# Performance work log

Measured on AMD Instinct MI355X. Metric: run time of the kernel, lower is better.

## Reference

```python
import jax, jax.numpy as jnp
import numpy as np

B, T, C = 48, 200, 53          # batch, timepoints, ICA components
E, H, A = 32, 64, 64            # embed dim, GRU hidden dim, attention hidden dim
C2 = C * C                      # 2809
E1 = round(0.05 * C2)           # gta_embed out = 140
E2 = round(0.5 * C2)            # gta_attend hidden = 1404
O = 2                           # output classes
BN_EPS = 1e-5


def setup_inputs() -> dict:
    key = jax.random.key(0)
    ks = jax.random.split(key, 24)
    n = lambda k, shape, s: jax.random.normal(k, shape, dtype=jnp.float32) * s
    return {
        "x": jax.random.normal(ks[0], (B, T, C), dtype=jnp.float32),
        "emb_w": n(ks[1], (E,), 0.3), "emb_b": n(ks[2], (E,), 0.1),
        "w_ih": n(ks[3], (3 * H, E), 0.12), "w_hh": n(ks[4], (3 * H, H), 0.12),
        "b_ih": n(ks[5], (3 * H,), 0.05), "b_hh": n(ks[6], (3 * H,), 0.05),
        "wq": n(ks[7], (A, H), 0.12), "bq": n(ks[8], (A,), 0.05),
        "wk": n(ks[9], (A, H), 0.12), "bk": n(ks[10], (A,), 0.05),
        "wv": n(ks[11], (H, H), 0.12), "bv": n(ks[12], (H,), 0.05),
        "u0": jax.random.normal(ks[13], (H,), dtype=jnp.float32),
        "w_g1": n(ks[14], (E1, C2), 0.02), "b_g1": n(ks[15], (E1,), 0.02),
        "bn_g": jnp.ones((E1,), jnp.float32), "bn_b": jnp.zeros((E1,), jnp.float32),
        "w_g2": n(ks[16], (E2, E1), 0.05), "b_g2": n(ks[17], (E2,), 0.05),
        "w_g3": n(ks[18], (1, E2), 0.02), "b_g3": n(ks[19], (1,), 0.02),
        "w_clf": n(ks[20], (O, C2), 0.02), "b_clf": jnp.zeros((O,), jnp.float32),
    }


def _normalize(v, eps=1e-12):
    return v / (jnp.linalg.norm(v) + eps)


def _gru_cell(x, h, w_ih, w_hh, b_ih, b_hh):
    # torch GRU cell math. x:(N,E) h:(N,H)
    gi = x @ w_ih.T + b_ih
    gh = h @ w_hh.T + b_hh
    i_r, i_z, i_n = jnp.split(gi, 3, axis=-1)
    h_r, h_z, h_n = jnp.split(gh, 3, axis=-1)
    r = jax.nn.sigmoid(i_r + h_r)
    z = jax.nn.sigmoid(i_z + h_z)
    n = jnp.tanh(i_n + r * h_n)
    return (1.0 - z) * n + z * h


def _forward(x, emb_w, emb_b, w_ih, w_hh, b_ih, b_hh, wq, bq, wk, bk, wv, bv, u0,
             w_g1, b_g1, bn_g, bn_b, w_g2, b_g2, w_g3, b_g3, w_clf, b_clf):
    Bs, Ts, Cs = x.shape
    Hd = wv.shape[0]
    # single shared Linear(1,E) embedding: (B,T,C) -> (T,B,C,E) for scan
    emb = x[..., None] * emb_w + emb_b
    emb = jnp.transpose(emb, (1, 0, 2, 3))
    h0 = jnp.zeros((Bs * Cs, Hd), x.dtype)

    def step(carry, emb_t):
        h, u = carry
        hg = _gru_cell(emb_t.reshape(Bs * Cs, -1), h, w_ih, w_hh, b_ih, b_hh)
        hb = hg.reshape(Bs, Cs, Hd)
        # spectral_norm on value weight: 5 power iterations (no_grad, as torch)
        v = None
        for _ in range(5):
            v = _normalize(wv.T @ u)
            u = _normalize(wv @ v)
        u = jax.lax.stop_gradient(u)
        v = jax.lax.stop_gradient(v)
        sigma = u @ (wv @ v)
        q = hb @ wq.T + bq          # (B,C,A)
        k = hb @ wk.T + bk          # (B,C,A)
        val = hb @ (wv / sigma).T + bv  # (B,C,H)
        scores = jnp.einsum('bia,bja->bij', q, k)  # (B,C,C)
        # eigenvalue-based spectral normalization (detached: track_grads=False)
        ev = jnp.linalg.eigvals(jax.lax.stop_gradient(scores))
        m = jnp.max(jnp.abs(ev), axis=1)[:, None, None].astype(x.dtype)
        attn = scores / m
        h_new = jnp.einsum('bij,bjh->bih', attn, val).reshape(Bs * Cs, Hd)
        return (h_new, u), attn

    (_, _), aligns = jax.lax.scan(step, (h0, u0), emb)  # aligns: (T,B,C,C)
    align = jnp.transpose(aligns, (1, 0, 2, 3))         # (B,T,C,C)
    Aflat = align.reshape(Bs, Ts, Cs * Cs)

    # gta_attention over the time axis
    xr = Aflat * Aflat.mean(axis=1, keepdims=True)
    flat = xr.reshape(Bs * Ts, Cs * Cs)
    e = flat @ w_g1.T + b_g1
    mu = e.mean(axis=0)
    var = e.var(axis=0)  # biased, as torch BatchNorm1d (training)
    e = jax.nn.relu((e - mu) / jnp.sqrt(var + BN_EPS) * bn_g + bn_b)
    a = jax.nn.relu(e @ w_g2.T + b_g2) @ w_g3.T + b_g3   # (B*T,1)
    a = jax.nn.softmax(a.reshape(Bs, Ts), axis=1)
    dnc = (Aflat * a[..., None]).sum(axis=1)             # (B,C*C)
    logits = dnc @ w_clf.T + b_clf
    return logits, dnc.reshape(Bs, Cs, Cs), align


def reference(x, emb_w, emb_b, w_ih, w_hh, b_ih, b_hh, wq, bq, wk, bk, wv, bv, u0,
              w_g1, b_g1, bn_g, bn_b, w_g2, b_g2, w_g3, b_g3, w_clf, b_clf):
    return _forward(x, emb_w, emb_b, w_ih, w_hh, b_ih, b_hh, wq, bq, wk, bk, wv, bv, u0,
                    w_g1, b_g1, bn_g, bn_b, w_g2, b_g2, w_g3, b_g3, w_clf, b_clf)
```

## Files before the change

kernel.cpp:

```cpp
#include <hip/hip_runtime.h>
#include <hip/hip_bf16.h>
#include <math.h>

#define B_  48
#define T_  200
#define C_  53
#define H_  64
#define C2_ 2809
#define E1_ 140
#define E2_ 1404
#define TS  60

typedef long long i64;

struct __align__(16) F4 { float v[4]; };
struct __align__(8)  F2 { float v[2]; };

__device__ __forceinline__ float wredsum(float v){
  #pragma unroll
  for (int o = 32; o > 0; o >>= 1) v += __shfl_xor(v, o);
  return v;
}
__device__ __forceinline__ float sigm(float x){ return 1.f/(1.f + __expf(-x)); }
__device__ __forceinline__ float tanhx(float x){
  float a = fabsf(x);
  float e = __expf(-2.f*a);
  float t = (1.f - e)/(1.f + e);
  return copysignf(t, x);
}

__device__ __forceinline__ void eig_mm(const float* __restrict__ X, float* __restrict__ Y,
                                       int r0, int c0, float inv,
                                       float& essq, float& etrc){
  float ea0[4] = {0.f,0.f,0.f,0.f};
  float ea1[4] = {0.f,0.f,0.f,0.f};
  for (int kq = 0; kq < 13; kq++){
    int k4 = kq*4;
    F4 a0 = *(const F4*)&X[(r0+0)*TS + k4];
    F4 a1 = *(const F4*)&X[(r0+1)*TS + k4];
    F4 b0 = *(const F4*)&X[(k4+0)*TS + c0];
    F4 b1 = *(const F4*)&X[(k4+1)*TS + c0];
    F4 b2 = *(const F4*)&X[(k4+2)*TS + c0];
    F4 b3 = *(const F4*)&X[(k4+3)*TS + c0];
    #pragma unroll
    for (int ci = 0; ci < 4; ci++){
      ea0[ci] += a0.v[0]*b0.v[ci] + a0.v[1]*b1.v[ci] + a0.v[2]*b2.v[ci] + a0.v[3]*b3.v[ci];
      ea1[ci] += a1.v[0]*b0.v[ci] + a1.v[1]*b1.v[ci] + a1.v[2]*b2.v[ci] + a1.v[3]*b3.v[ci];
    }
  }
  {
    float a0 = X[(r0+0)*TS + 52], a1 = X[(r0+1)*TS + 52];
    F4 bb = *(const F4*)&X[52*TS + c0];
    #pragma unroll
    for (int ci = 0; ci < 4; ci++){ ea0[ci] += a0*bb.v[ci]; ea1[ci] += a1*bb.v[ci]; }
  }
  F4 o0, o1;
  #pragma unroll
  for (int ci = 0; ci < 4; ci++){
    o0.v[ci] = ea0[ci]*inv;
    o1.v[ci] = ea1[ci]*inv;
    essq += o0.v[ci]*o0.v[ci] + o1.v[ci]*o1.v[ci];
  }
  if (r0   >= c0 && r0   < c0+4) etrc += o0.v[r0-c0];
  if (r0+1 >= c0 && r0+1 < c0+4) etrc += o1.v[r0+1-c0];
  *(F4*)&Y[(r0+0)*TS + c0] = o0;
  *(F4*)&Y[(r0+1)*TS + c0] = o1;
}

#define OFF_SIGMA 0
#define OFF_WHHT  200
#define OFF_WZV   12488
#define OFF_WUV   20680
#define OFF_P     20812
#define OFF_R0    21004
#define OFF_MM    21196
#define OFF_M2    25292
#define OFF_M4    29388
#define OFF_M5    33484
#define OFF_AMEAN 37580
#define OFF_E     172412
#define OFF_CA    1516412
#define OFF_CB    1516552
#define OFF_APRE  1516692
#define OFF_A     1526292
#define OFF_G2T   1535892

__global__ void k_prep1(const float* __restrict__ w_hh, const float* __restrict__ wq,
                        const float* __restrict__ wk, const float* __restrict__ wv,
                        const float* __restrict__ w_ih, const float* __restrict__ emb_w,
                        const float* __restrict__ emb_b, const float* __restrict__ b_ih,
                        const float* __restrict__ bq, const float* __restrict__ bk,
                        const float* __restrict__ w_g2,
                        float* whhT, float* wzv, float* wuv, float* g2t,
                        float* p, float* r0){
  int idx0 = blockIdx.x*blockDim.x + threadIdx.x;
  int stride = gridDim.x*blockDim.x;
  for (int i = idx0; i < 64*192; i += stride){
    int kk = i/192, g = i%192;
    whhT[i] = w_hh[g*64 + kk];
  }
  for (int i = idx0; i < 8192; i += stride){
    int h = i >> 7, a = i & 127;
    if (a < 64){
      float g = 0.f;
      for (int m = 0; m < 64; m++) g += wq[m*64 + h]*wk[m*64 + a];
      wzv[i] = g;
    } else {
      wzv[i] = wv[(a-64)*64 + h];
    }
  }
  for (int i = idx0; i < 129; i += stride){
    if (i < 64){
      float s = 0.f;
      for (int m = 0; m < 64; m++) s += wq[m*64 + i]*bk[m];
      wuv[i] = s;
    } else if (i < 128){
      int h = i - 64;
      float s = 0.f;
      for (int m = 0; m < 64; m++) s += wk[m*64 + h]*bq[m];
      wuv[i] = s;
    } else {
      float s = 0.f;
      for (int m = 0; m < 64; m++) s += bq[m]*bk[m];
      wuv[128] = s;
    }
  }
  for (int i = idx0; i < 140*1404; i += stride){ int k = i/1404, n = i%1404; g2t[i] = w_g2[n*140+k]; }
  for (int i = idx0; i < 192; i += stride){
    float s1 = 0.f, s2 = 0.f;
    for (int e = 0; e < 32; e++){ float w = w_ih[i*32+e]; s1 += w*emb_w[e]; s2 += w*emb_b[e]; }
    p[i] = s1; r0[i] = s2 + b_ih[i];
  }
}

__global__ void k_prep2(const float* __restrict__ wv, const float* __restrict__ u0,
                        float* Wm, float* Wm2, float* Wm4, float* Wm5, float* sigma){
  int r = threadIdx.x;
  for (int c = 0; c < 64; c++){
    float s = 0.f;
    for (int k = 0; k < 64; k++) s += wv[r*64+k]*wv[c*64+k];
    Wm[r*64+c] = s;
  }
  __syncthreads();
  for (int c = 0; c < 64; c++){
    float s = 0.f;
    for (int k = 0; k < 64; k++) s += Wm[r*64+k]*Wm[k*64+c];
    Wm2[r*64+c] = s;
  }
  __syncthreads();
  for (int c = 0; c < 64; c++){
    float s = 0.f;
    for (int k = 0; k < 64; k++) s += Wm2[r*64+k]*Wm2[k*64+c];
    Wm4[r*64+c] = s;
  }
  __syncthreads();
  for (int c = 0; c < 64; c++){
    float s = 0.f;
    for (int k = 0; k < 64; k++) s += Wm4[r*64+k]*Wm[k*64+c];
    Wm5[r*64+c] = s;
  }
  __syncthreads();
  __shared__ float su[64];
  su[r] = u0[r];
  __syncthreads();
  for (int t = 0; t < T_; t++){
    float z = 0.f, w = 0.f;
    for (int k = 0; k < 64; k++){ float uk = su[k]; z += Wm4[r*64+k]*uk; w += Wm5[r*64+k]*uk; }
    float nw = wredsum(w*w);
    float zw = wredsum(z*w);
    float sg = sqrtf(nw / fmaxf(zw, 1e-35f));
    if (r == 0) sigma[t] = sg;
    float wn = w * (1.f/sqrtf(fmaxf(nw, 1e-35f)));
    __syncthreads();
    su[r] = wn;
    __syncthreads();
  }
}

__global__ __launch_bounds__(512, 1) void k_scan(
    const float* __restrict__ x, const float* __restrict__ b_hh,
    const float* __restrict__ bv,
    const float* __restrict__ whhT, const float* __restrict__ wzv,
    const float* __restrict__ wuv,
    const float* __restrict__ wp, const float* __restrict__ wr0,
    const float* __restrict__ sigma, float* __restrict__ outAL){
  __shared__ __align__(16) float L[19056];
  float* Rh  = L;
  float* R4  = L + 3840;
  float* R3  = L + 7680;
  float* R2  = L + 11520;
  float* R1  = L + 14912;
  float* Lp  = L + 18272;
  float* Lr0 = L + 18464;
  float* Lbh = L + 18656;
  float* Lbv = L + 18848;
  float* Lrq = L + 18912;
  float* Lrk = L + 18968;
  float* Lsc = L + 19024;
  int tid = threadIdx.x;
  int b = blockIdx.x;

  for (int i = tid; i < 192; i += 512){ Lp[i] = wp[i]; Lr0[i] = wr0[i]; Lbh[i] = b_hh[i]; }
  for (int i = tid; i < 64; i += 512) Lbv[i] = bv[i];
  for (int i = tid; i < 18272; i += 512) L[i] = 0.f;
  __syncthreads();

  int ct4 = tid >> 4, jt4 = tid & 15;
  int c0g = ct4*4, j0g = jt4*4;
  int it14 = tid/14, jt14 = tid%14;
  int i0s = it14*4, j0s = jt14*4;
  int ctq = tid >> 5, gtq = tid & 31;
  int c0q = ctq*4, g0q = gtq*4;
  int erg = tid/14, ecg = tid%14;
  int er0 = erg*2, ec0 = ecg*4;

  const float c0v = wuv[128];

  for (int t = 0; t < T_; t++){
    if (tid < 32) Lsc[tid] = 0.f;
    if (tid < 224){
      float gacc[3][4][4];
      #pragma unroll
      for (int g = 0; g < 3; g++)
        #pragma unroll
        for (int ji = 0; ji < 4; ji++){
          float bb = Lbh[g*64 + j0g + ji];
          #pragma unroll
          for (int ci = 0; ci < 4; ci++) gacc[g][ji][ci] = bb;
        }
      for (int kk = 0; kk < 64; kk++){
        F4 hv = *(F4*)&Rh[kk*TS + c0g];
        F4 w0 = *(const F4*)&whhT[kk*192 + j0g];
        F4 w1 = *(const F4*)&whhT[kk*192 + 64 + j0g];
        F4 w2 = *(const F4*)&whhT[kk*192 + 128 + j0g];
        #pragma unroll
        for (int ji = 0; ji < 4; ji++)
          #pragma unroll
          for (int ci = 0; ci < 4; ci++){
            gacc[0][ji][ci] += hv.v[ci]*w0.v[ji];
            gacc[1][ji][ci] += hv.v[ci]*w1.v[ji];
            gacc[2][ji][ci] += hv.v[ci]*w2.v[ji];
          }
      }
      float xv[4];
      #pragma unroll
      for (int ci = 0; ci < 4; ci++){
        int c = c0g + ci;
        xv[ci] = (c < C_) ? x[(i64)(b*T_ + t)*C_ + c] : 0.f;
      }
      F4 p0 = *(F4*)&Lp[j0g], p1 = *(F4*)&Lp[64+j0g], p2 = *(F4*)&Lp[128+j0g];
      F4 q0 = *(F4*)&Lr0[j0g], q1 = *(F4*)&Lr0[64+j0g], q2 = *(F4*)&Lr0[128+j0g];
      #pragma unroll
      for (int ji = 0; ji < 4; ji++){
        F4 hold = *(F4*)&Rh[(j0g+ji)*TS + c0g];
        F4 o;
        #pragma unroll
        for (int ci = 0; ci < 4; ci++){
          float rr = sigm(xv[ci]*p0.v[ji] + q0.v[ji] + gacc[0][ji][ci]);
          float zz = sigm(xv[ci]*p1.v[ji] + q1.v[ji] + gacc[1][ji][ci]);
          float nn = tanhx(xv[ci]*p2.v[ji] + q2.v[ji] + rr*gacc[2][ji][ci]);
          float hg = (1.f - zz)*nn + zz*hold.v[ci];
          o.v[ci] = (c0g + ci < C_) ? hg : 0.f;
        }
        *(F4*)&R4[(j0g+ji)*TS + c0g] = o;
      }
    }
    __syncthreads();
    if (tid < 448){
      float acc[4][4];
      #pragma unroll
      for (int gi = 0; gi < 4; gi++)
        #pragma unroll
        for (int ci = 0; ci < 4; ci++) acc[gi][ci] = 0.f;
      for (int kk = 0; kk < 64; kk++){
        F4 a = *(F4*)&R4[kk*TS + c0q];
        F4 w = *(const F4*)&wzv[kk*128 + g0q];
        #pragma unroll
        for (int gi = 0; gi < 4; gi++)
          #pragma unroll
          for (int ci = 0; ci < 4; ci++) acc[gi][ci] += a.v[ci]*w.v[gi];
      }
      if (g0q < 64){
        #pragma unroll
        for (int gi = 0; gi < 4; gi++){
          F4 o;
          #pragma unroll
          for (int ci = 0; ci < 4; ci++) o.v[ci] = acc[gi][ci];
          *(F4*)&R3[(g0q+gi)*TS + c0q] = o;
        }
      } else {
        float invs = 1.f/sigma[t];
        int a0i = g0q - 64;
        #pragma unroll
        for (int ci = 0; ci < 4; ci++){
          int c = c0q + ci;
          if (c < C_){
            F4 o;
            #pragma unroll
            for (int gi = 0; gi < 4; gi++) o.v[gi] = acc[gi][ci]*invs + Lbv[a0i+gi];
            *(F4*)&R2[c*64 + a0i] = o;
          }
        }
      }
    } else if (tid < 504){
      int u = tid - 448;
      float rq = 0.f, rk = 0.f;
      if (u < C_){
        for (int h = 0; h < 64; h++){
          float hv = R4[h*TS + u];
          rq += hv*wuv[h];
          rk += hv*wuv[64+h];
        }
      }
      if (u < 56){ Lrq[u] = rq; Lrk[u] = rk; }
    }
    __syncthreads();
    {
      float sacc[4][4];
      float ssq = 0.f, trc = 0.f;
      if (tid < 196){
        #pragma unroll
        for (int ii = 0; ii < 4; ii++)
          #pragma unroll
          for (int jj = 0; jj < 4; jj++){
            int i = i0s + ii, j = j0s + jj;
            sacc[ii][jj] = (i < C_ && j < C_) ? (Lrq[i] + Lrk[j] + c0v) : 0.f;
          }
        for (int aq = 0; aq < 16; aq++){
          int a4 = aq*4;
          F4 qa0 = *(F4*)&R3[(a4+0)*TS + i0s];
          F4 qa1 = *(F4*)&R3[(a4+1)*TS + i0s];
          F4 qa2 = *(F4*)&R3[(a4+2)*TS + i0s];
          F4 qa3 = *(F4*)&R3[(a4+3)*TS + i0s];
          F4 kb0 = *(F4*)&R4[(a4+0)*TS + j0s];
          F4 kb1 = *(F4*)&R4[(a4+1)*TS + j0s];
          F4 kb2 = *(F4*)&R4[(a4+2)*TS + j0s];
          F4 kb3 = *(F4*)&R4[(a4+3)*TS + j0s];
          #pragma unroll
          for (int ii = 0; ii < 4; ii++)
            #pragma unroll
            for (int jj = 0; jj < 4; jj++)
              sacc[ii][jj] += qa0.v[ii]*kb0.v[jj] + qa1.v[ii]*kb1.v[jj]
                            + qa2.v[ii]*kb2.v[jj] + qa3.v[ii]*kb3.v[jj];
        }
        #pragma unroll
        for (int ii = 0; ii < 4; ii++){
          int i = i0s + ii;
          if (i < C_){
            F4 o;
            #pragma unroll
            for (int jj = 0; jj < 4; jj++){
              o.v[jj] = sacc[ii][jj];
              ssq += sacc[ii][jj]*sacc[ii][jj];
            }
            *(F4*)&R1[i*TS + j0s] = o;
            if (j0s <= i && i < j0s + 4) trc += sacc[ii][i - j0s];
          }
        }
      }
      ssq = wredsum(ssq); trc = wredsum(trc);
      if ((tid & 63) == 0){
        if (ssq != 0.f) atomicAdd(&Lsc[0], ssq);
        if (trc != 0.f) atomicAdd(&Lsc[1], trc);
      }
    }
    __syncthreads();
    {
      float inv0 = 1.f/fmaxf(Lsc[0], 1e-35f);
      float essq = 0.f, etrc = 0.f;
      if (tid < 378) eig_mm(R1, R3, er0, ec0, inv0, essq, etrc);
      essq = wredsum(essq); etrc = wredsum(etrc);
      if ((tid & 63) == 0){
        if (essq != 0.f) atomicAdd(&Lsc[2], essq);
        if (etrc != 0.f) atomicAdd(&Lsc[3], etrc);
      }
    }
    __syncthreads();
    float Gacc = 0.f, prevest = 1e30f, est = 0.f;
    int cnt = 0;
    float pssq = fmaxf(Lsc[0], 1e-35f), ptr1 = Lsc[1];
    float* Xb = R3; float* Yb = R4;
    for (int j = 2; j <= 13; j++){
      float sj = fmaxf(Lsc[2*(j-1)], 1e-35f);
      float tj = Lsc[2*(j-1)+1];
      int J = j - 2;
      float t1n = ptr1/sqrtf(pssq);
      float t2n = tj;
      float disc = 2.f*t2n - t1n*t1n;
      float rq = (disc >= 0.f) ? 0.5f*(fabsf(t1n) + sqrtf(disc))
                               : sqrtf(fmaxf(0.5f*(t1n*t1n - t2n), 1e-30f));
      rq = fminf(fmaxf(rq, 0.02f), 1.5f);
      est = Gacc + ldexpf(0.5f*log2f(pssq) + log2f(rq), -J);
      if (fabsf(est - prevest) < 1e-4f) cnt++; else cnt = 0;
      prevest = est;
      Gacc += ldexpf(log2f(pssq), -(J+1));
      if ((J >= 4 && cnt >= 1) || j == 13) break;
      pssq = sj; ptr1 = tj;
      {
        float inv = 1.f/sj;
        float essq = 0.f, etrc = 0.f;
        if (tid < 378) eig_mm(Xb, Yb, er0, ec0, inv, essq, etrc);
        essq = wredsum(essq); etrc = wredsum(etrc);
        if ((tid & 63) == 0){
          if (essq != 0.f) atomicAdd(&Lsc[2*j], essq);
          if (etrc != 0.f) atomicAdd(&Lsc[2*j+1], etrc);
        }
      }
      { float* tp = Xb; Xb = Yb; Yb = tp; }
      __syncthreads();
    }
    float invm = exp2f(-est);
    if (tid < 224){
      float hraw0[4] = {0.f,0.f,0.f,0.f};
      float hraw1[4] = {0.f,0.f,0.f,0.f};
      float hraw2[4] = {0.f,0.f,0.f,0.f};
      float hraw3[4] = {0.f,0.f,0.f,0.f};
      for (int kq = 0; kq < 13; kq++){
        int k4 = kq*4;
        F4 a0 = *(F4*)&R1[(c0g+0)*TS + k4];
        F4 a1 = *(F4*)&R1[(c0g+1)*TS + k4];
        F4 a2 = *(F4*)&R1[(c0g+2)*TS + k4];
        F4 a3 = *(F4*)&R1[(c0g+3)*TS + k4];
        F4 b0 = *(F4*)&R2[(k4+0)*64 + j0g];
        F4 b1 = *(F4*)&R2[(k4+1)*64 + j0g];
        F4 b2 = *(F4*)&R2[(k4+2)*64 + j0g];
        F4 b3 = *(F4*)&R2[(k4+3)*64 + j0g];
        #pragma unroll
        for (int jj = 0; jj < 4; jj++){
          hraw0[jj] += a0.v[0]*b0.v[jj] + a0.v[1]*b1.v[jj] + a0.v[2]*b2.v[jj] + a0.v[3]*b3.v[jj];
          hraw1[jj] += a1.v[0]*b0.v[jj] + a1.v[1]*b1.v[jj] + a1.v[2]*b2.v[jj] + a1.v[3]*b3.v[jj];
          hraw2[jj] += a2.v[0]*b0.v[jj] + a2.v[1]*b1.v[jj] + a2.v[2]*b2.v[jj] + a2.v[3]*b3.v[jj];
          hraw3[jj] += a3.v[0]*b0.v[jj] + a3.v[1]*b1.v[jj] + a3.v[2]*b2.v[jj] + a3.v[3]*b3.v[jj];
        }
      }
      {
        const int k = 52;
        float a0 = R1[(c0g+0)*TS + k], a1 = R1[(c0g+1)*TS + k];
        float a2 = R1[(c0g+2)*TS + k], a3 = R1[(c0g+3)*TS + k];
        F4 bb = *(F4*)&R2[k*64 + j0g];
        #pragma unroll
        for (int jj = 0; jj < 4; jj++){
          hraw0[jj] += a0*bb.v[jj];
          hraw1[jj] += a1*bb.v[jj];
          hraw2[jj] += a2*bb.v[jj];
          hraw3[jj] += a3*bb.v[jj];
        }
      }
      #pragma unroll
      for (int jj = 0; jj < 4; jj++){
        F4 o;
        o.v[0] = (c0g + 0 < C_) ? hraw0[jj]*invm : 0.f;
        o.v[1] = (c0g + 1 < C_) ? hraw1[jj]*invm : 0.f;
        o.v[2] = (c0g + 2 < C_) ? hraw2[jj]*invm : 0.f;
        o.v[3] = (c0g + 3 < C_) ? hraw3[jj]*invm : 0.f;
        *(F4*)&Rh[(j0g+jj)*TS + c0g] = o;
      }
    } else if (tid < 420){
      int u = tid - 224;
      int i0 = (u/14)*4, j0 = (u%14)*4;
      float* ALrow = outAL + (i64)(b*T_ + t)*C2_;
      #pragma unroll
      for (int ii = 0; ii < 4; ii++){
        int i = i0 + ii;
        if (i < C_){
          F4 s = *(F4*)&R1[i*TS + j0];
          #pragma unroll
          for (int jj = 0; jj < 4; jj++){
            int jc = j0 + jj;
            if (jc < C_) ALrow[i*C_ + jc] = s.v[jj]*invm;
          }
        }
      }
    }
    __syncthreads();
  }
}

__global__ void k_amean(const float* __restrict__ AL, float* __restrict__ amean){
  int b = blockIdx.x/11, ch = blockIdx.x%11;
  int c2 = ch*256 + threadIdx.x;
  if (c2 >= C2_) return;
  float acc = 0.f;
  for (int t = 0; t < T_; t++)
    acc += AL[(i64)(b*T_ + t)*C2_ + c2];
  amean[(i64)b*C2_ + c2] = acc*(1.f/(float)T_);
}

__global__ __launch_bounds__(256) void k_gemm1(const float* __restrict__ AL,
                                               const float* __restrict__ amean,
                                               const float* __restrict__ w_g1,
                                               float* __restrict__ e){
  __shared__ __align__(16) float At[64][68];
  __shared__ __align__(16) float Bt[64][148];
  int mt = blockIdx.x >> 2, ks = blockIdx.x & 3;
  int tid = threadIdx.x;
  float acc[4][10];
  #pragma unroll
  for (int ri = 0; ri < 4; ri++)
    #pragma unroll
    for (int ci = 0; ci < 10; ci++) acc[ri][ci] = 0.f;
  int rg = tid/14, cg = tid%14;
  int r0 = rg*4, cc0 = cg*10;
  for (int kb = 0; kb < 11; kb++){
    int k0 = (ks*11 + kb)*64;
    for (int idx = tid; idx < 4096; idx += 256){
      int r = idx >> 6, i = idx & 63;
      int kk = k0 + i;
      int row = mt*64 + r, bb = row/T_;
      float v = 0.f;
      if (kk < C2_) v = AL[(i64)row*C2_ + kk]*amean[(i64)bb*C2_ + kk];
      At[i][r] = v;
    }
    for (int idx = tid; idx < 9216; idx += 256){
      int c = idx >> 6, i = idx & 63;
      int kk = k0 + i;
      float v = 0.f;
      if (c < E1_ && kk < C2_) v = w_g1[(i64)c*C2_ + kk];
      Bt[i][c] = v;
    }
    __syncthreads();
    if (tid < 224){
      for (int i = 0; i < 64; i++){
        F4 a = *(F4*)&At[i][r0];
        float bv[10];
        #pragma unroll
        for (int u = 0; u < 5; u++){
          F2 b2 = *(F2*)&Bt[i][cc0 + u*2];
          bv[u*2] = b2.v[0]; bv[u*2+1] = b2.v[1];
        }
        #pragma unroll
        for (int ri = 0; ri < 4; ri++)
          #pragma unroll
          for (int ci = 0; ci < 10; ci++)
            acc[ri][ci] += a.v[ri]*bv[ci];
      }
    }
    __syncthreads();
  }
  if (tid < 224){
    #pragma unroll
    for (int ri = 0; ri < 4; ri++)
      #pragma unroll
      for (int ci = 0; ci < 10; ci++){
        int c = cc0 + ci;
        if (c < E1_) atomicAdd(&e[(i64)(mt*64 + r0 + ri)*E1_ + c], acc[ri][ci]);
      }
  }
}

__global__ void k_bnstats(const float* __restrict__ e, const float* __restrict__ bn_g,
                          const float* __restrict__ bn_b, float* cA, float* cB){
  __shared__ float s1a[256], s2a[256];
  int c = blockIdx.x, tid = threadIdx.x;
  float s1 = 0.f, s2 = 0.f;
  for (int row = tid; row < B_*T_; row += 256){
    float v = e[(i64)row*E1_ + c];
    s1 += v; s2 += v*v;
  }
  s1a[tid] = s1; s2a[tid] = s2; __syncthreads();
  for (int s = 128; s > 0; s >>= 1){
    if (tid < s){ s1a[tid] += s1a[tid+s]; s2a[tid] += s2a[tid+s]; }
    __syncthreads();
  }
  if (tid == 0){
    float n = (float)(B_*T_);
    float mu = s1a[0]/n;
    float var = s2a[0]/n - mu*mu;
    float a = bn_g[c]/sqrtf(var + 1e-5f);
    cA[c] = a; cB[c] = bn_b[c] - mu*a;
  }
}

__global__ __launch_bounds__(128) void k_gemm2(const float* __restrict__ e,
                                               const float* __restrict__ cA, const float* __restrict__ cB,
                                               const float* __restrict__ g2t,
                                               const float* __restrict__ b_g2, const float* __restrict__ w_g3,
                                               float* __restrict__ apre){
  __shared__ __align__(16) float At2[140][68];
  int mt = blockIdx.x/30, nc = blockIdx.x%30;
  int tid = threadIdx.x;
  int nbase = nc*48;
  for (int idx = tid; idx < 64*140; idx += 128){
    int r = idx/140, k = idx - r*140;
    float v = e[(i64)(mt*64 + r)*E1_ + k]*cA[k] + cB[k];
    At2[k][r] = fmaxf(v, 0.f);
  }
  __syncthreads();
  if (tid < 96){
    int rg = tid/6, ng = tid%6;
    int r0 = rg*4, n0 = nbase + ng*8;
    float acc[4][8];
    #pragma unroll
    for (int ri = 0; ri < 4; ri++)
      #pragma unroll
      for (int ni = 0; ni < 8; ni++) acc[ri][ni] = 0.f;
    for (int k = 0; k < E1_; k++){
      F4 a = *(F4*)&At2[k][r0];
      float bvv[8];
      if (n0 + 8 <= E2_){
        F4 b0 = *(const F4*)&g2t[(i64)k*E2_ + n0];
        F4 b1 = *(const F4*)&g2t[(i64)k*E2_ + n0 + 4];
        #pragma unroll
        for (int u = 0; u < 4; u++){ bvv[u] = b0.v[u]; bvv[u+4] = b1.v[u]; }
      } else {
        #pragma unroll
        for (int ni = 0; ni < 8; ni++){ int n = n0+ni; bvv[ni] = (n < E2_) ? g2t[(i64)k*E2_ + n] : 0.f; }
      }
      #pragma unroll
      for (int ri = 0; ri < 4; ri++)
        #pragma unroll
        for (int ni = 0; ni < 8; ni++) acc[ri][ni] += a.v[ri]*bvv[ni];
    }
    #pragma unroll
    for (int ri = 0; ri < 4; ri++){
      float s = 0.f;
      #pragma unroll
      for (int ni = 0; ni < 8; ni++){
        int n = n0 + ni;
        if (n < E2_){
          float a2 = acc[ri][ni] + b_g2[n];
          if (a2 > 0.f) s += a2*w_g3[n];
        }
      }
      atomicAdd(&apre[mt*64 + r0 + ri], s);
    }
  }
}

__global__ void k_soft(const float* __restrict__ apre, const float* __restrict__ b_clf,
                       float* __restrict__ wa, float* __restrict__ out){
  __shared__ float sr[256];
  int b = blockIdx.x, tid = threadIdx.x;
  float v = (tid < T_) ? apre[b*T_ + tid] : -3.4e38f;
  sr[tid] = v; __syncthreads();
  for (int s = 128; s > 0; s >>= 1){ if (tid < s) sr[tid] = fmaxf(sr[tid], sr[tid+s]); __syncthreads(); }
  float mx = sr[0]; __syncthreads();
  float ev = (tid < T_) ? __expf(v - mx) : 0.f;
  sr[tid] = ev; __syncthreads();
  for (int s = 128; s > 0; s >>= 1){ if (tid < s) sr[tid] += sr[tid+s]; __syncthreads(); }
  float den = sr[0];
  if (tid < T_) wa[b*T_ + tid] = ev/den;
  if (b == 0 && tid < 2*B_) out[tid] = b_clf[tid & 1];
}

__global__ void k_dnc(const float* __restrict__ AL, const float* __restrict__ wa,
                      const float* __restrict__ w_clf, float* __restrict__ out){
  int b = blockIdx.x/11, ch = blockIdx.x%11;
  int c2 = ch*256 + threadIdx.x;
  float acc = 0.f;
  if (c2 < C2_){
    for (int t = 0; t < T_; t++)
      acc += AL[(i64)(b*T_ + t)*C2_ + c2]*wa[b*T_ + t];
    out[96 + (i64)b*C2_ + c2] = acc;
  }
  float p0 = (c2 < C2_) ? acc*w_clf[c2]        : 0.f;
  float p1 = (c2 < C2_) ? acc*w_clf[C2_ + c2]  : 0.f;
  p0 = wredsum(p0); p1 = wredsum(p1);
  if ((threadIdx.x & 63) == 0){
    atomicAdd(&out[b*2 + 0], p0);
    atomicAdd(&out[b*2 + 1], p1);
  }
}

extern "C" void kernel_launch(void* const* d_in, const int* in_sizes, int n_in,
                              void* d_out, int out_size, void* d_ws, size_t ws_size,
                              hipStream_t stream){
  const float* x     = (const float*)d_in[0];
  const float* emb_w = (const float*)d_in[1];
  const float* emb_b = (const float*)d_in[2];
  const float* w_ih  = (const float*)d_in[3];
  const float* w_hh  = (const float*)d_in[4];
  const float* b_ih  = (const float*)d_in[5];
  const float* b_hh  = (const float*)d_in[6];
  const float* wq    = (const float*)d_in[7];
  const float* bq    = (const float*)d_in[8];
  const float* wk    = (const float*)d_in[9];
  const float* bk    = (const float*)d_in[10];
  const float* wv_in = (const float*)d_in[11];
  const float* bv    = (const float*)d_in[12];
  const float* u0    = (const float*)d_in[13];
  const float* w_g1  = (const float*)d_in[14];
  const float* bn_g  = (const float*)d_in[16];
  const float* bn_b  = (const float*)d_in[17];
  const float* w_g2  = (const float*)d_in[18];
  const float* b_g2  = (const float*)d_in[19];
  const float* w_g3  = (const float*)d_in[20];
  const float* w_clf = (const float*)d_in[22];
  const float* b_clf = (const float*)d_in[23];
  float* out = (float*)d_out;
  float* W = (float*)d_ws;

  float* wsig   = W + OFF_SIGMA;
  float* whhT   = W + OFF_WHHT;
  float* wzv    = W + OFF_WZV;
  float* wuv    = W + OFF_WUV;
  float* wp     = W + OFF_P;
  float* wr0    = W + OFF_R0;
  float* wM     = W + OFF_MM;
  float* wM2    = W + OFF_M2;
  float* wM4    = W + OFF_M4;
  float* wM5    = W + OFF_M5;
  float* wamean = W + OFF_AMEAN;
  float* we     = W + OFF_E;
  float* wcA    = W + OFF_CA;
  float* wcB    = W + OFF_CB;
  float* wapre  = W + OFF_APRE;
  float* wa     = W + OFF_A;
  float* wg2t   = W + OFF_G2T;

  float* outAL = out + 96 + (i64)B_*C2_;

  hipMemsetAsync(we, 0, (size_t)(B_*T_)*E1_*sizeof(float), stream);
  hipMemsetAsync(wapre, 0, (size_t)(B_*T_)*sizeof(float), stream);

  k_prep1<<<96, 256, 0, stream>>>(w_hh, wq, wk, wv_in, w_ih, emb_w, emb_b, b_ih, bq, bk,
                                  w_g2, whhT, wzv, wuv, wg2t, wp, wr0);
  k_prep2<<<1, 64, 0, stream>>>(wv_in, u0, wM, wM2, wM4, wM5, wsig);
  k_scan<<<B_, 512, 0, stream>>>(x, b_hh, bv, whhT, wzv, wuv, wp, wr0, wsig, outAL);
  k_amean<<<B_*11, 256, 0, stream>>>(outAL, wamean);
  k_gemm1<<<600, 256, 0, stream>>>(outAL, wamean, w_g1, we);
  k_bnstats<<<E1_, 256, 0, stream>>>(we, bn_g, bn_b, wcA, wcB);
  k_gemm2<<<150*30, 128, 0, stream>>>(we, wcA, wcB, wg2t, b_g2, w_g3, wapre);
  k_soft<<<B_, 256, 0, stream>>>(wapre, b_clf, wa, out);
  k_dnc<<<B_*11, 256, 0, stream>>>(outAL, wa, w_clf, out);
}
```

Baseline: 8.720 ms.

## Overlap unscaled attention-value matmul with first eigen-step and loosen convergence check

The first eigen squaring matmul is remapped to 252 threads with 3x4 tiles. The freed threads run the attention-times-value product (R1·R2) concurrently, before the normalising scale is known, and that product is later rescaled in place by invm. This takes the value matmul off the serial path after the log-norm iteration. The convergence test now allows an early break one iteration sooner (J>=3), which saves an eigen step but may slightly change the estimate's accuracy.

```diff
diff --git a/kernel.cpp b/kernel.cpp
--- a/kernel.cpp
+++ b/kernel.cpp
@@ -65,6 +65,52 @@
   if (r0+1 >= c0 && r0+1 < c0+4) etrc += o1.v[r0+1-c0];
   *(F4*)&Y[(r0+0)*TS + c0] = o0;
   *(F4*)&Y[(r0+1)*TS + c0] = o1;
+}
+
+__device__ __forceinline__ void eig_mm3(const float* __restrict__ X, float* __restrict__ Y,
+                                        int r0, int c0, float inv,
+                                        float& essq, float& etrc){
+  float ea0[4] = {0.f,0.f,0.f,0.f};
+  float ea1[4] = {0.f,0.f,0.f,0.f};
+  float ea2[4] = {0.f,0.f,0.f,0.f};
+  for (int kq = 0; kq < 13; kq++){
+    int k4 = kq*4;
+    F4 a0 = *(const F4*)&X[(r0+0)*TS + k4];
+    F4 a1 = *(const F4*)&X[(r0+1)*TS + k4];
+    F4 a2 = *(const F4*)&X[(r0+2)*TS + k4];
+    F4 b0 = *(const F4*)&X[(k4+0)*TS + c0];
+    F4 b1 = *(const F4*)&X[(k4+1)*TS + c0];
+    F4 b2 = *(const F4*)&X[(k4+2)*TS + c0];
+    F4 b3 = *(const F4*)&X[(k4+3)*TS + c0];
+    #pragma unroll
+    for (int ci = 0; ci < 4; ci++){
+      ea0[ci] += a0.v[0]*b0.v[ci] + a0.v[1]*b1.v[ci] + a0.v[2]*b2.v[ci] + a0.v[3]*b3.v[ci];
+      ea1[ci] += a1.v[0]*b0.v[ci] + a1.v[1]*b1.v[ci] + a1.v[2]*b2.v[ci] + a1.v[3]*b3.v[ci];
+      ea2[ci] += a2.v[0]*b0.v[ci] + a2.v[1]*b1.v[ci] + a2.v[2]*b2.v[ci] + a2.v[3]*b3.v[ci];
+    }
+  }
+  {
+    float a0 = X[(r0+0)*TS + 52], a1 = X[(r0+1)*TS + 52], a2 = X[(r0+2)*TS + 52];
+    F4 bb = *(const F4*)&X[52*TS + c0];
+    #pragma unroll
+    for (int ci = 0; ci < 4; ci++){
+      ea0[ci] += a0*bb.v[ci]; ea1[ci] += a1*bb.v[ci]; ea2[ci] += a2*bb.v[ci];
+    }
+  }
+  F4 o0, o1, o2;
+  #pragma unroll
+  for (int ci = 0; ci < 4; ci++){
+    o0.v[ci] = ea0[ci]*inv;
+    o1.v[ci] = ea1[ci]*inv;
+    o2.v[ci] = ea2[ci]*inv;
+    essq += o0.v[ci]*o0.v[ci] + o1.v[ci]*o1.v[ci] + o2.v[ci]*o2.v[ci];
+  }
+  if (r0   >= c0 && r0   < c0+4) etrc += o0.v[r0-c0];
+  if (r0+1 >= c0 && r0+1 < c0+4) etrc += o1.v[r0+1-c0];
+  if (r0+2 >= c0 && r0+2 < c0+4) etrc += o2.v[r0+2-c0];
+  *(F4*)&Y[(r0+0)*TS + c0] = o0;
+  *(F4*)&Y[(r0+1)*TS + c0] = o1;
+  *(F4*)&Y[(r0+2)*TS + c0] = o2;
 }
 
 #define OFF_SIGMA 0
@@ -366,9 +412,59 @@
     }
     __syncthreads();
     {
-      float inv0 = 1.f/fmaxf(Lsc[0], 1e-35f);
       float essq = 0.f, etrc = 0.f;
-      if (tid < 378) eig_mm(R1, R3, er0, ec0, inv0, essq, etrc);
+      if (tid < 252){
+        float inv0 = 1.f/fmaxf(Lsc[0], 1e-35f);
+        int r0e = (tid/14)*3, c0e = (tid%14)*4;
+        eig_mm3(R1, R3, r0e, c0e, inv0, essq, etrc);
+      } else if (tid < 476){
+        int u = tid - 252;
+        int c0 = (u >> 4)*4, j0 = (u & 15)*4;
+        float hr0[4] = {0.f,0.f,0.f,0.f};
+        float hr1[4] = {0.f,0.f,0.f,0.f};
+        float hr2[4] = {0.f,0.f,0.f,0.f};
+        float hr3[4] = {0.f,0.f,0.f,0.f};
+        for (int kq = 0; kq < 13; kq++){
+          int k4 = kq*4;
+          F4 a0 = *(F4*)&R1[(c0+0)*TS + k4];
+          F4 a1 = *(F4*)&R1[(c0+1)*TS + k4];
+          F4 a2 = *(F4*)&R1[(c0+2)*TS + k4];
+          F4 a3 = *(F4*)&R1[(c0+3)*TS + k4];
+          F4 b0 = *(F4*)&R2[(k4+0)*64 + j0];
+          F4 b1 = *(F4*)&R2[(k4+1)*64 + j0];
+          F4 b2 = *(F4*)&R2[(k4+2)*64 + j0];
+          F4 b3 = *(F4*)&R2[(k4+3)*64 + j0];
+          #pragma unroll
+          for (int jj = 0; jj < 4; jj++){
+            hr0[jj] += a0.v[0]*b0.v[jj] + a0.v[1]*b1.v[jj] + a0.v[2]*b2.v[jj] + a0.v[3]*b3.v[jj];
+            hr1[jj] += a1.v[0]*b0.v[jj] + a1.v[1]*b1.v[jj] + a1.v[2]*b2.v[jj] + a1.v[3]*b3.v[jj];
+            hr2[jj] += a2.v[0]*b0.v[jj] + a2.v[1]*b1.v[jj] + a2.v[2]*b2.v[jj] + a2.v[3]*b3.v[jj];
+            hr3[jj] += a3.v[0]*b0.v[jj] + a3.v[1]*b1.v[jj] + a3.v[2]*b2.v[jj] + a3.v[3]*b3.v[jj];
+          }
+        }
+        {
+          const int k = 52;
+          float a0 = R1[(c0+0)*TS + k], a1 = R1[(c0+1)*TS + k];
+          float a2 = R1[(c0+2)*TS + k], a3 = R1[(c0+3)*TS + k];
+          F4 bb = *(F4*)&R2[k*64 + j0];
+          #pragma unroll
+          for (int jj = 0; jj < 4; jj++){
+            hr0[jj] += a0*bb.v[jj];
+            hr1[jj] += a1*bb.v[jj];
+            hr2[jj] += a2*bb.v[jj];
+            hr3[jj] += a3*bb.v[jj];
+          }
+        }
+        #pragma unroll
+        for (int jj = 0; jj < 4; jj++){
+          F4 o;
+          o.v[0] = (c0 + 0 < C_) ? hr0[jj] : 0.f;
+          o.v[1] = (c0 + 1 < C_) ? hr1[jj] : 0.f;
+          o.v[2] = (c0 + 2 < C_) ? hr2[jj] : 0.f;
+          o.v[3] = (c0 + 3 < C_) ? hr3[jj] : 0.f;
+          *(F4*)&Rh[(j0+jj)*TS + c0] = o;
+        }
+      }
       essq = wredsum(essq); etrc = wredsum(etrc);
       if ((tid & 63) == 0){
         if (essq != 0.f) atomicAdd(&Lsc[2], essq);
@@ -394,7 +490,7 @@
       if (fabsf(est - prevest) < 1e-4f) cnt++; else cnt = 0;
       prevest = est;
       Gacc += ldexpf(log2f(pssq), -(J+1));
-      if ((J >= 4 && cnt >= 1) || j == 13) break;
+      if ((J >= 3 && cnt >= 1) || j == 13) break;
       pssq = sj; ptr1 = tj;
       {
         float inv = 1.f/sj;
@@ -411,49 +507,11 @@
     }
     float invm = exp2f(-est);
     if (tid < 224){
-      float hraw0[4] = {0.f,0.f,0.f,0.f};
-      float hraw1[4] = {0.f,0.f,0.f,0.f};
-      float hraw2[4] = {0.f,0.f,0.f,0.f};
-      float hraw3[4] = {0.f,0.f,0.f,0.f};
-      for (int kq = 0; kq < 13; kq++){
-        int k4 = kq*4;
-        F4 a0 = *(F4*)&R1[(c0g+0)*TS + k4];
-        F4 a1 = *(F4*)&R1[(c0g+1)*TS + k4];
-        F4 a2 = *(F4*)&R1[(c0g+2)*TS + k4];
-        F4 a3 = *(F4*)&R1[(c0g+3)*TS + k4];
-        F4 b0 = *(F4*)&R2[(k4+0)*64 + j0g];
-        F4 b1 = *(F4*)&R2[(k4+1)*64 + j0g];
-        F4 b2 = *(F4*)&R2[(k4+2)*64 + j0g];
-        F4 b3 = *(F4*)&R2[(k4+3)*64 + j0g];
-        #pragma unroll
-        for (int jj = 0; jj < 4; jj++){
-          hraw0[jj] += a0.v[0]*b0.v[jj] + a0.v[1]*b1.v[jj] + a0.v[2]*b2.v[jj] + a0.v[3]*b3.v[jj];
-          hraw1[jj] += a1.v[0]*b0.v[jj] + a1.v[1]*b1.v[jj] + a1.v[2]*b2.v[jj] + a1.v[3]*b3.v[jj];
-          hraw2[jj] += a2.v[0]*b0.v[jj] + a2.v[1]*b1.v[jj] + a2.v[2]*b2.v[jj] + a2.v[3]*b3.v[jj];
-          hraw3[jj] += a3.v[0]*b0.v[jj] + a3.v[1]*b1.v[jj] + a3.v[2]*b2.v[jj] + a3.v[3]*b3.v[jj];
-        }
-      }
-      {
-        const int k = 52;
-        float a0 = R1[(c0g+0)*TS + k], a1 = R1[(c0g+1)*TS + k];
-        float a2 = R1[(c0g+2)*TS + k], a3 = R1[(c0g+3)*TS + k];
-        F4 bb = *(F4*)&R2[k*64 + j0g];
-        #pragma unroll
-        for (int jj = 0; jj < 4; jj++){
-          hraw0[jj] += a0*bb.v[jj];
-          hraw1[jj] += a1*bb.v[jj];
-          hraw2[jj] += a2*bb.v[jj];
-          hraw3[jj] += a3*bb.v[jj];
-        }
-      }
-      #pragma unroll
-      for (int jj = 0; jj < 4; jj++){
-        F4 o;
-        o.v[0] = (c0g + 0 < C_) ? hraw0[jj]*invm : 0.f;
-        o.v[1] = (c0g + 1 < C_) ? hraw1[jj]*invm : 0.f;
-        o.v[2] = (c0g + 2 < C_) ? hraw2[jj]*invm : 0.f;
-        o.v[3] = (c0g + 3 < C_) ? hraw3[jj]*invm : 0.f;
-        *(F4*)&Rh[(j0g+jj)*TS + c0g] = o;
+      for (int idx = tid; idx < 960; idx += 224){
+        F4 v = *(F4*)&Rh[idx*4];
+        #pragma unroll
+        for (int u = 0; u < 4; u++) v.v[u] *= invm;
+        *(F4*)&Rh[idx*4] = v;
       }
     } else if (tid < 420){
       int u = tid - 224;
```

After: 10.11 ms. 1.16x slower.
